# Kernel tuning notes

Hardware: AMD Instinct MI355X
Metric: run time of the kernel (lower is better)

The kernel has to match this reference:

```python
import jax, jax.numpy as jnp
import numpy as np

N = 8192      # nodes
E = 262144    # edges (avg degree 32)
D = 128       # embed dim
F = 128       # input feature dim
H = 128       # GCN hidden
C = 7         # classes
EPS = 1e-4    # sample_bias for concrete noise


def setup_inputs() -> dict:
    key = jax.random.key(0)
    ks = jax.random.split(key, 10)
    x = jax.random.normal(ks[0], (N, F), jnp.float32)
    embed = jax.random.normal(ks[1], (N, D), jnp.float32)
    row = jax.random.randint(ks[2], (E,), 0, N, jnp.int64)
    col = jax.random.randint(ks[3], (E,), 0, N, jnp.int64)
    adj_data = jnp.ones((E,), jnp.float32)
    # uniform noise in (bias, 1-bias) as in concrete_sample(training=True)
    noise = jax.random.uniform(ks[4], (E,), jnp.float32, EPS, 1.0 - EPS)
    tmp = jnp.ones((1,), jnp.float32)  # temperature beta
    W1e = jax.random.normal(ks[5], (3 * D, 64), jnp.float32) * 0.05
    b1e = jnp.zeros((64,), jnp.float32)
    W2e = jax.random.normal(ks[6], (64, 1), jnp.float32) * 0.05
    b2e = jnp.zeros((1,), jnp.float32)
    Wg0 = jax.random.normal(ks[7], (F, H), jnp.float32) * 0.05
    Wg1 = jax.random.normal(ks[8], (H, C), jnp.float32) * 0.05
    return {"x": x, "embed": embed, "adj_data": adj_data, "noise": noise,
            "tmp": tmp, "W1e": W1e, "b1e": b1e, "W2e": W2e, "b2e": b2e,
            "Wg0": Wg0, "Wg1": Wg1, "row": row, "col": col, "nodeid": 5}


def reference(x, embed, adj_data, noise, tmp, W1e, b1e, W2e, b2e, Wg0, Wg1,
              row, col, nodeid):
    # gather node embeddings per edge + self node embedding, concat -> [E, 3D]
    f1 = embed[row]
    f2 = embed[col]
    selfemb = jnp.broadcast_to(embed[nodeid][None, :], (f1.shape[0], D))
    f12self = jnp.concatenate([f1, f2, selfemb], axis=-1)
    # 2-layer explainer MLP -> per-edge logit
    h = jax.nn.relu(f12self @ W1e + b1e)
    log_alpha = (h @ W2e + b2e).reshape(-1)  # [E]
    # concrete-sigmoid reparameterization (training=True path, noise supplied)
    gate_inputs = (jnp.log(noise) - jnp.log1p(-noise) + log_alpha) / tmp[0]
    values = jax.nn.sigmoid(gate_inputs)
    # scatter edge gates and adjacency values into dense [N, N]
    mask = jnp.zeros((N, N), jnp.float32).at[row, col].add(values)
    adj = jnp.zeros((N, N), jnp.float32).at[row, col].add(adj_data)
    # symmetrize mask, apply to adjacency, zero the diagonal
    sym_mask = (mask + mask.T) * 0.5
    masked_adj = adj * sym_mask * (1.0 - jnp.eye(N, dtype=jnp.float32))
    # wrapped GNN: 2-layer GCN
    h1 = jax.nn.relu(masked_adj @ (x @ Wg0))
    out = masked_adj @ (h1 @ Wg1)
    node_pred = out[nodeid]  # [C]
    return jax.nn.softmax(node_pred, axis=0)
```

## Files before the change

kernel.cpp:

```cpp
#include <hip/hip_runtime.h>
#include <hip/hip_bf16.h>
#include <math.h>

#define NNODES 8192
#define DIM 128
#define SMAX 128
#define HSIZE 16384
#define LDAT 136
#define LDW 68

__device__ __forceinline__ int detect64(const void* rowp) {
    const long long* p = (const long long*)rowp;
    int is64 = 1;
#pragma unroll
    for (int i = 0; i < 4; i++) {
        long long v = p[i];
        if (v < 0 || v >= NNODES) is64 = 0;
    }
    return is64;
}

__device__ __forceinline__ int edge_idx(const void* p, int e, int idx64) {
    if (idx64) return (int)((const long long*)p)[e];
    return ((const int*)p)[e];
}

__device__ __forceinline__ int hash_insert(unsigned int* hashK, unsigned int key1) {
    unsigned int h = (key1 * 2654435761u) & (HSIZE - 1);
    for (;;) {
        unsigned int prev = atomicCAS(&hashK[h], 0u, key1);
        if (prev == 0u || prev == key1) return (int)h;
        h = (h + 1) & (HSIZE - 1);
    }
}


__global__ __launch_bounds__(256) void k_zero(float4* z, int n4) {
    int i = blockIdx.x * blockDim.x + threadIdx.x;
    if (i < n4) z[i] = make_float4(0.f, 0.f, 0.f, 0.f);
}

__global__ __launch_bounds__(512) void k_dense(
        const float* embed, const float* x, const float* W1e, const float* b1e,
        const float* Wg0, const int* nodep, const void* rowp, const void* colp,
        const float* adjd,
        float* U, float* V, float* xw, float* cself,
        int* flags, float* cnt0, int* nbr, int* slotmap, int E) {
    int bid = blockIdx.x;
    int t = threadIdx.x;
    int nodeid = nodep[0];
    int tile = bid >> 1;
    int colh = bid & 1;

    __shared__ float At[128 * LDAT];
    __shared__ float Wl[128 * LDW];
    __shared__ float semb[DIM];

    const float* Asrc = (tile < 64) ? embed + (size_t)tile * 128 * DIM
                                    : x + (size_t)(tile - 64) * 128 * DIM;
    for (int i = t; i < 128 * DIM; i += 512)
        At[(i & 127) * LDAT + (i >> 7)] = Asrc[i];
    if (tile < 64) {
        int doff = colh * 128;
        for (int i = t; i < 128 * 64; i += 512)
            Wl[(i >> 6) * LDW + (i & 63)] = W1e[(size_t)(doff + (i >> 6)) * 64 + (i & 63)];
    } else {
        for (int i = t; i < 128 * 64; i += 512)
            Wl[(i >> 6) * LDW + (i & 63)] = Wg0[(size_t)(i >> 6) * DIM + colh * 64 + (i & 63)];
    }
    if (bid == 0 && t < DIM) semb[t] = embed[(size_t)nodeid * DIM + t];
    __syncthreads();

    int rg = t & 31;
    int cg = t >> 5;
    float acc[4][4];
#pragma unroll
    for (int i = 0; i < 4; i++)
#pragma unroll
        for (int j = 0; j < 4; j++) acc[i][j] = 0.f;

#pragma unroll 4
    for (int d = 0; d < DIM; d++) {
        float4 a4 = *(const float4*)&At[d * LDAT + rg * 4];
        float4 w4 = *(const float4*)&Wl[d * LDW + cg * 4];
        const float* ap = &a4.x;
        const float* wp = &w4.x;
#pragma unroll
        for (int i = 0; i < 4; i++)
#pragma unroll
            for (int j = 0; j < 4; j++)
                acc[i][j] = fmaf(ap[i], wp[j], acc[i][j]);
    }

    if (tile < 64) {
        float* o = colh ? V : U;
        int n0 = tile * 128;
#pragma unroll
        for (int i = 0; i < 4; i++)
            *(float4*)&o[(size_t)(n0 + rg * 4 + i) * 64 + cg * 4] =
                make_float4(acc[i][0], acc[i][1], acc[i][2], acc[i][3]);
    } else {
        int n0 = (tile - 64) * 128;
#pragma unroll
        for (int i = 0; i < 4; i++)
            *(float4*)&xw[(size_t)(n0 + rg * 4 + i) * DIM + colh * 64 + cg * 4] =
                make_float4(acc[i][0], acc[i][1], acc[i][2], acc[i][3]);
    }

    if (bid == 0 && t < 64) {
        float a = b1e[t];
        for (int d = 0; d < DIM; d++)
            a += semb[d] * W1e[(size_t)(2 * DIM + d) * 64 + t];
        cself[t] = a;
    }

    int idx64 = detect64(rowp);
    for (int e = bid * 512 + t; e < E; e += 256 * 512) {
        int r = edge_idx(rowp, e, idx64);
        if (r != nodeid) continue;
        int c = edge_idx(colp, e, idx64);
        if (c == nodeid) continue;
        atomicAdd(&cnt0[c], adjd[e]);
        if (atomicCAS((unsigned int*)&slotmap[c], 0u, 0xFFFFFFFFu) == 0u) {
            int s = atomicAdd(&flags[1], 1);
            if (s < SMAX) {
                nbr[s] = c;
                __hip_atomic_store(&slotmap[c], s + 1, __ATOMIC_RELAXED,
                                   __HIP_MEMORY_SCOPE_AGENT);
            }
        }
    }
}

__global__ __launch_bounds__(1024) void k_gates(
        const float* adjd, const float* noise, const float* tmp,
        const float* W2e, const float* b2e,
        const void* rowp, const void* colp, const int* nodep,
        const float* U, const float* V, const float* cself,
        const int* slotmap,
        unsigned int* hashK, float* hashC, float* hashF, float* hashR,
        float* f0s, float* r0s, int E) {
    int idx64 = detect64(rowp);
    int nodeid = nodep[0];
    int e = blockIdx.x * blockDim.x + threadIdx.x;
    if (e >= E) return;
    int r = edge_idx(rowp, e, idx64);
    int c = edge_idx(colp, e, idx64);
    if (r == c) return;
    int spr = slotmap[r];
    int spc = slotmap[c];
    bool fr = spr > 0, fc = spc > 0;
    if (!fr && !fc) return;
    float la = b2e[0];
    const float4* u4 = (const float4*)(U + (size_t)r * 64);
    const float4* v4 = (const float4*)(V + (size_t)c * 64);
    const float4* c4 = (const float4*)cself;
    const float4* w4 = (const float4*)W2e;
#pragma unroll
    for (int d = 0; d < 16; d++) {
        float4 uu = u4[d], vv = v4[d], cc = c4[d], ww = w4[d];
        float h0 = uu.x + vv.x + cc.x;
        float h1 = uu.y + vv.y + cc.y;
        float h2 = uu.z + vv.z + cc.z;
        float h3 = uu.w + vv.w + cc.w;
        la += (h0 > 0.f ? h0 : 0.f) * ww.x + (h1 > 0.f ? h1 : 0.f) * ww.y
            + (h2 > 0.f ? h2 : 0.f) * ww.z + (h3 > 0.f ? h3 : 0.f) * ww.w;
    }
    float nz = noise[e];
    float gi = (logf(nz) - log1pf(-nz) + la) / tmp[0];
    float v = 1.f / (1.f + expf(-gi));
    if (fr) {
        int sr = spr - 1;
        unsigned int key1 = ((unsigned int)(sr << 13) | (unsigned int)c) + 1u;
        int idx = hash_insert(hashK, key1);
        atomicAdd(&hashC[idx], adjd[e]);
        atomicAdd(&hashF[idx], v);
        if (c == nodeid) atomicAdd(&r0s[sr], v);
    }
    if (fc) {
        int sc = spc - 1;
        unsigned int key1 = ((unsigned int)(sc << 13) | (unsigned int)r) + 1u;
        int idx = hash_insert(hashK, key1);
        atomicAdd(&hashR[idx], v);
        if (r == nodeid) atomicAdd(&f0s[sc], v);
    }
}

__global__ __launch_bounds__(1024) void k_hagg(
        const unsigned int* hashK, const float* hashC, const float* hashF,
        const float* hashR, const float* xw, float* h1acc) {
    int gid = blockIdx.x * blockDim.x + threadIdx.x;
    int group = gid >> 7;
    int tg = gid & 127;
    int ngroups = (256 * 1024) >> 7;
    for (int entry = group; entry < HSIZE; entry += ngroups) {
        unsigned int key1 = hashK[entry];
        if (key1 == 0u) continue;
        float wgt = hashC[entry] * (hashF[entry] + hashR[entry]) * 0.5f;
        if (wgt == 0.f) continue;
        unsigned int key = key1 - 1u;
        int s = (int)(key >> 13);
        int k = (int)(key & 8191u);
        atomicAdd(&h1acc[(size_t)s * DIM + tg], wgt * xw[(size_t)k * DIM + tg]);
    }
}

__global__ __launch_bounds__(1024) void k_final(
        const int* flags, const float* h1acc, const float* cnt0, const int* nbr,
        const float* f0s, const float* r0s, const float* Wg1, float* out) {
    int t = threadIdx.x;
    __shared__ float sacc[7];
    if (t < 7) sacc[t] = 0.f;
    __syncthreads();
    int ns = flags[1]; if (ns > SMAX) ns = SMAX;
    int wave = t >> 6, lane = t & 63;
    for (int s = wave; s < ns; s += 16) {
        float a0 = cnt0[nbr[s]] * (f0s[s] + r0s[s]) * 0.5f;
        float v0 = h1acc[(size_t)s * DIM + lane];
        float v1 = h1acc[(size_t)s * DIM + lane + 64];
        v0 = v0 > 0.f ? v0 : 0.f;
        v1 = v1 > 0.f ? v1 : 0.f;
        float part[7];
        for (int c = 0; c < 7; c++) {
            float p = v0 * Wg1[lane * 7 + c] + v1 * Wg1[(lane + 64) * 7 + c];
            for (int o = 32; o >= 1; o >>= 1) p += __shfl_xor(p, o, 64);
            part[c] = p;
        }
        if (lane == 0)
            for (int c = 0; c < 7; c++) atomicAdd(&sacc[c], a0 * part[c]);
    }
    __syncthreads();
    if (t == 0) {
        float v[7], m = -1e30f, ssum = 0.f;
        for (int c = 0; c < 7; c++) { v[c] = sacc[c]; if (v[c] > m) m = v[c]; }
        for (int c = 0; c < 7; c++) { v[c] = expf(v[c] - m); ssum += v[c]; }
        for (int c = 0; c < 7; c++) out[c] = v[c] / ssum;
    }
}

extern "C" void kernel_launch(void* const* d_in, const int* in_sizes, int n_in,
                              void* d_out, int out_size, void* d_ws, size_t ws_size,
                              hipStream_t stream) {
    const float* x     = (const float*)d_in[0];
    const float* embed = (const float*)d_in[1];
    const float* adjd  = (const float*)d_in[2];
    const float* noise = (const float*)d_in[3];
    const float* tmp   = (const float*)d_in[4];
    const float* W1e   = (const float*)d_in[5];
    const float* b1e   = (const float*)d_in[6];
    const float* W2e   = (const float*)d_in[7];
    const float* b2e   = (const float*)d_in[8];
    const float* Wg0   = (const float*)d_in[9];
    const float* Wg1   = (const float*)d_in[10];
    const void*  rowp  = d_in[11];
    const void*  colp  = d_in[12];
    const int*   nodep = (const int*)d_in[13];
    int E = in_sizes[3];

    char* w = (char*)d_ws;
    size_t off = 0;
    auto alloc = [&](size_t bytes) -> char* {
        char* p = w + off;
        off = (off + bytes + 255) & ~(size_t)255;
        return p;
    };
    float*        cself   = (float*)alloc(64 * 4);
    int*          nbr     = (int*)  alloc(SMAX * 4);
    float*        U       = (float*)alloc((size_t)NNODES * 64 * 4);
    float*        V       = (float*)alloc((size_t)NNODES * 64 * 4);
    float*        xw      = (float*)alloc((size_t)NNODES * DIM * 4);
    char*         zstart  = w + off;
    int*          flags   = (int*)  alloc(256);
    int*          slotmap = (int*)  alloc((size_t)NNODES * 4);
    float*        cnt0    = (float*)alloc((size_t)NNODES * 4);
    float*        f0s     = (float*)alloc(SMAX * 4);
    float*        r0s     = (float*)alloc(SMAX * 4);
    unsigned int* hashK   = (unsigned int*)alloc((size_t)HSIZE * 4);
    float*        hashC   = (float*)alloc((size_t)HSIZE * 4);
    float*        hashF   = (float*)alloc((size_t)HSIZE * 4);
    float*        hashR   = (float*)alloc((size_t)HSIZE * 4);
    float*        h1acc   = (float*)alloc((size_t)SMAX * DIM * 4);
    size_t zbytes  = (size_t)((w + off) - zstart);
    int n4 = (int)(zbytes / 16);

    k_zero<<<(n4 + 255) / 256, 256, 0, stream>>>((float4*)zstart, n4);
    k_dense<<<256, 512, 0, stream>>>(embed, x, W1e, b1e, Wg0, nodep, rowp, colp,
                                     adjd, U, V, xw, cself, flags, cnt0, nbr,
                                     slotmap, E);
    k_gates<<<E / 1024, 1024, 0, stream>>>(adjd, noise, tmp, W2e, b2e,
                                           rowp, colp, nodep, U, V, cself,
                                           slotmap, hashK, hashC, hashF, hashR,
                                           f0s, r0s, E);
    k_hagg<<<256, 1024, 0, stream>>>(hashK, hashC, hashF, hashR, xw, h1acc);
    k_final<<<1, 1024, 0, stream>>>(flags, h1acc, cnt0, nbr, f0s, r0s, Wg1,
                                    (float*)d_out);
}
```

Before: 49.33 us.

## Aggregate raw features before Wg0 projection and parallelize final GCN layer

Instead of computing x@Wg0 for all 8192 nodes up front, the hash aggregation now sums raw x rows per neighbor slot, and the final kernel applies Wg0 only to the at most 128 aggregated rows, using one block per slot. This uses linearity to avoid a full dense projection and halves the dense kernel's tile work, which now only computes the explainer U/V with smaller blocks. The hash tables and the aggregation buffer are zeroed inside the dense kernel rather than by k_zero. A last-block-done counter performs the final softmax, which adds a grid-wide atomic handshake.

Measured after the change: 48.21 us. 2.3% less time.

```diff
diff --git a/kernel.cpp b/kernel.cpp
--- a/kernel.cpp
+++ b/kernel.cpp
@@ -6,8 +6,7 @@
 #define DIM 128
 #define SMAX 128
 #define HSIZE 16384
-#define LDAT 136
-#define LDW 68
+#define LDA2 68
 
 __device__ __forceinline__ int detect64(const void* rowp) {
     const long long* p = (const long long*)rowp;
@@ -40,39 +39,36 @@
     if (i < n4) z[i] = make_float4(0.f, 0.f, 0.f, 0.f);
 }
 
-__global__ __launch_bounds__(512) void k_dense(
-        const float* embed, const float* x, const float* W1e, const float* b1e,
-        const float* Wg0, const int* nodep, const void* rowp, const void* colp,
-        const float* adjd,
-        float* U, float* V, float* xw, float* cself,
-        int* flags, float* cnt0, int* nbr, int* slotmap, int E) {
+__global__ __launch_bounds__(256) void k_dense(
+        const float* embed, const float* W1e, const float* b1e,
+        const int* nodep, const void* rowp, const void* colp, const float* adjd,
+        float* U, float* V, float* cself,
+        int* flags, float* cnt0, int* nbr, int* slotmap,
+        float* hzero, int nhz, int E) {
     int bid = blockIdx.x;
     int t = threadIdx.x;
+    int gid = bid * 256 + t;
     int nodeid = nodep[0];
     int tile = bid >> 1;
     int colh = bid & 1;
 
-    __shared__ float At[128 * LDAT];
-    __shared__ float Wl[128 * LDW];
+    __shared__ float At[128 * LDA2];
+    __shared__ float Wl[128 * LDA2];
     __shared__ float semb[DIM];
 
-    const float* Asrc = (tile < 64) ? embed + (size_t)tile * 128 * DIM
-                                    : x + (size_t)(tile - 64) * 128 * DIM;
-    for (int i = t; i < 128 * DIM; i += 512)
-        At[(i & 127) * LDAT + (i >> 7)] = Asrc[i];
-    if (tile < 64) {
-        int doff = colh * 128;
-        for (int i = t; i < 128 * 64; i += 512)
-            Wl[(i >> 6) * LDW + (i & 63)] = W1e[(size_t)(doff + (i >> 6)) * 64 + (i & 63)];
-    } else {
-        for (int i = t; i < 128 * 64; i += 512)
-            Wl[(i >> 6) * LDW + (i & 63)] = Wg0[(size_t)(i >> 6) * DIM + colh * 64 + (i & 63)];
-    }
+    for (int i = gid; i < nhz; i += 256 * 256) hzero[i] = 0.f;
+
+    const float* Asrc = embed + (size_t)tile * 64 * DIM;
+    for (int i = t; i < 64 * DIM; i += 256)
+        At[(i & 127) * LDA2 + (i >> 7)] = Asrc[i];
+    int doff = colh * 128;
+    for (int i = t; i < 128 * 64; i += 256)
+        Wl[(i >> 6) * LDA2 + (i & 63)] = W1e[(size_t)(doff + (i >> 6)) * 64 + (i & 63)];
     if (bid == 0 && t < DIM) semb[t] = embed[(size_t)nodeid * DIM + t];
     __syncthreads();
 
-    int rg = t & 31;
-    int cg = t >> 5;
+    int rg = t & 15;
+    int cg = t >> 4;
     float acc[4][4];
 #pragma unroll
     for (int i = 0; i < 4; i++)
@@ -81,8 +77,8 @@
 
 #pragma unroll 4
     for (int d = 0; d < DIM; d++) {
-        float4 a4 = *(const float4*)&At[d * LDAT + rg * 4];
-        float4 w4 = *(const float4*)&Wl[d * LDW + cg * 4];
+        float4 a4 = *(const float4*)&At[d * LDA2 + rg * 4];
+        float4 w4 = *(const float4*)&Wl[d * LDA2 + cg * 4];
         const float* ap = &a4.x;
         const float* wp = &w4.x;
 #pragma unroll
@@ -92,20 +88,12 @@
                 acc[i][j] = fmaf(ap[i], wp[j], acc[i][j]);
     }
 
-    if (tile < 64) {
-        float* o = colh ? V : U;
-        int n0 = tile * 128;
-#pragma unroll
-        for (int i = 0; i < 4; i++)
-            *(float4*)&o[(size_t)(n0 + rg * 4 + i) * 64 + cg * 4] =
-                make_float4(acc[i][0], acc[i][1], acc[i][2], acc[i][3]);
-    } else {
-        int n0 = (tile - 64) * 128;
-#pragma unroll
-        for (int i = 0; i < 4; i++)
-            *(float4*)&xw[(size_t)(n0 + rg * 4 + i) * DIM + colh * 64 + cg * 4] =
-                make_float4(acc[i][0], acc[i][1], acc[i][2], acc[i][3]);
-    }
+    float* o = colh ? V : U;
+    int n0 = tile * 64;
+#pragma unroll
+    for (int i = 0; i < 4; i++)
+        *(float4*)&o[(size_t)(n0 + rg * 4 + i) * 64 + cg * 4] =
+            make_float4(acc[i][0], acc[i][1], acc[i][2], acc[i][3]);
 
     if (bid == 0 && t < 64) {
         float a = b1e[t];
@@ -115,7 +103,7 @@
     }
 
     int idx64 = detect64(rowp);
-    for (int e = bid * 512 + t; e < E; e += 256 * 512) {
+    for (int e = gid; e < E; e += 256 * 256) {
         int r = edge_idx(rowp, e, idx64);
         if (r != nodeid) continue;
         int c = edge_idx(colp, e, idx64);
@@ -188,7 +176,7 @@
 
 __global__ __launch_bounds__(1024) void k_hagg(
         const unsigned int* hashK, const float* hashC, const float* hashF,
-        const float* hashR, const float* xw, float* h1acc) {
+        const float* hashR, const float* x, float* xagg) {
     int gid = blockIdx.x * blockDim.x + threadIdx.x;
     int group = gid >> 7;
     int tg = gid & 127;
@@ -201,41 +189,59 @@
         unsigned int key = key1 - 1u;
         int s = (int)(key >> 13);
         int k = (int)(key & 8191u);
-        atomicAdd(&h1acc[(size_t)s * DIM + tg], wgt * xw[(size_t)k * DIM + tg]);
-    }
-}
-
-__global__ __launch_bounds__(1024) void k_final(
-        const int* flags, const float* h1acc, const float* cnt0, const int* nbr,
-        const float* f0s, const float* r0s, const float* Wg1, float* out) {
-    int t = threadIdx.x;
-    __shared__ float sacc[7];
-    if (t < 7) sacc[t] = 0.f;
-    __syncthreads();
+        atomicAdd(&xagg[(size_t)s * DIM + tg], wgt * x[(size_t)k * DIM + tg]);
+    }
+}
+
+__global__ __launch_bounds__(128) void k_final(
+        const int* flags, const float* xagg, const float* cnt0, const int* nbr,
+        const float* f0s, const float* r0s, const float* Wg0, const float* Wg1,
+        float* glogits, int* done, float* out) {
+    int b = blockIdx.x, t = threadIdx.x;
     int ns = flags[1]; if (ns > SMAX) ns = SMAX;
-    int wave = t >> 6, lane = t & 63;
-    for (int s = wave; s < ns; s += 16) {
-        float a0 = cnt0[nbr[s]] * (f0s[s] + r0s[s]) * 0.5f;
-        float v0 = h1acc[(size_t)s * DIM + lane];
-        float v1 = h1acc[(size_t)s * DIM + lane + 64];
-        v0 = v0 > 0.f ? v0 : 0.f;
-        v1 = v1 > 0.f ? v1 : 0.f;
+    if (b < ns) {
+        __shared__ float xs[DIM];
+        __shared__ float pacc[2][7];
+        xs[t] = xagg[(size_t)b * DIM + t];
+        __syncthreads();
+        float h = 0.f;
+        for (int d = 0; d < DIM; d++) h = fmaf(xs[d], Wg0[d * DIM + t], h);
+        h = h > 0.f ? h : 0.f;
+        int wave = t >> 6, lane = t & 63;
         float part[7];
         for (int c = 0; c < 7; c++) {
-            float p = v0 * Wg1[lane * 7 + c] + v1 * Wg1[(lane + 64) * 7 + c];
+            float p = h * Wg1[t * 7 + c];
             for (int o = 32; o >= 1; o >>= 1) p += __shfl_xor(p, o, 64);
             part[c] = p;
         }
         if (lane == 0)
-            for (int c = 0; c < 7; c++) atomicAdd(&sacc[c], a0 * part[c]);
+            for (int c = 0; c < 7; c++) pacc[wave][c] = part[c];
+        __syncthreads();
+        if (t == 0) {
+            float a0 = cnt0[nbr[b]] * (f0s[b] + r0s[b]) * 0.5f;
+            for (int c = 0; c < 7; c++)
+                atomicAdd(&glogits[c * 16], a0 * (pacc[0][c] + pacc[1][c]));
+        }
     }
     __syncthreads();
+    __shared__ int lastb;
     if (t == 0) {
-        float v[7], m = -1e30f, ssum = 0.f;
-        for (int c = 0; c < 7; c++) { v[c] = sacc[c]; if (v[c] > m) m = v[c]; }
-        for (int c = 0; c < 7; c++) { v[c] = expf(v[c] - m); ssum += v[c]; }
-        for (int c = 0; c < 7; c++) out[c] = v[c] / ssum;
-    }
+        __threadfence();
+        int old = __hip_atomic_fetch_add(done, 1, __ATOMIC_ACQ_REL,
+                                         __HIP_MEMORY_SCOPE_AGENT);
+        lastb = (old == SMAX - 1) ? 1 : 0;
+    }
+    __syncthreads();
+    if (!lastb || t != 0) return;
+    __builtin_amdgcn_fence(__ATOMIC_ACQUIRE, "agent");
+    float v[7], m = -1e30f, ssum = 0.f;
+    for (int c = 0; c < 7; c++) {
+        v[c] = __hip_atomic_load(&glogits[c * 16], __ATOMIC_RELAXED,
+                                 __HIP_MEMORY_SCOPE_AGENT);
+        if (v[c] > m) m = v[c];
+    }
+    for (int c = 0; c < 7; c++) { v[c] = expf(v[c] - m); ssum += v[c]; }
+    for (int c = 0; c < 7; c++) out[c] = v[c] / ssum;
 }
 
 extern "C" void kernel_launch(void* const* d_in, const int* in_sizes, int n_in,
@@ -268,30 +274,32 @@
     int*          nbr     = (int*)  alloc(SMAX * 4);
     float*        U       = (float*)alloc((size_t)NNODES * 64 * 4);
     float*        V       = (float*)alloc((size_t)NNODES * 64 * 4);
-    float*        xw      = (float*)alloc((size_t)NNODES * DIM * 4);
     char*         zstart  = w + off;
     int*          flags   = (int*)  alloc(256);
+    float*        glogits = (float*)alloc(512);
     int*          slotmap = (int*)  alloc((size_t)NNODES * 4);
     float*        cnt0    = (float*)alloc((size_t)NNODES * 4);
     float*        f0s     = (float*)alloc(SMAX * 4);
     float*        r0s     = (float*)alloc(SMAX * 4);
+    size_t zbytes  = (size_t)((w + off) - zstart);
     unsigned int* hashK   = (unsigned int*)alloc((size_t)HSIZE * 4);
     float*        hashC   = (float*)alloc((size_t)HSIZE * 4);
     float*        hashF   = (float*)alloc((size_t)HSIZE * 4);
     float*        hashR   = (float*)alloc((size_t)HSIZE * 4);
-    float*        h1acc   = (float*)alloc((size_t)SMAX * DIM * 4);
-    size_t zbytes  = (size_t)((w + off) - zstart);
+    float*        xagg    = (float*)alloc((size_t)SMAX * DIM * 4);
+    int nhz = HSIZE * 4 + SMAX * DIM;
     int n4 = (int)(zbytes / 16);
 
     k_zero<<<(n4 + 255) / 256, 256, 0, stream>>>((float4*)zstart, n4);
-    k_dense<<<256, 512, 0, stream>>>(embed, x, W1e, b1e, Wg0, nodep, rowp, colp,
-                                     adjd, U, V, xw, cself, flags, cnt0, nbr,
-                                     slotmap, E);
+    k_dense<<<256, 256, 0, stream>>>(embed, W1e, b1e, nodep, rowp, colp, adjd,
+                                     U, V, cself, flags, cnt0, nbr, slotmap,
+                                     (float*)hashK, nhz, E);
     k_gates<<<E / 1024, 1024, 0, stream>>>(adjd, noise, tmp, W2e, b2e,
                                            rowp, colp, nodep, U, V, cself,
                                            slotmap, hashK, hashC, hashF, hashR,
                                            f0s, r0s, E);
-    k_hagg<<<256, 1024, 0, stream>>>(hashK, hashC, hashF, hashR, xw, h1acc);
-    k_final<<<1, 1024, 0, stream>>>(flags, h1acc, cnt0, nbr, f0s, r0s, Wg1,
-                                    (float*)d_out);
-}
+    k_hagg<<<256, 1024, 0, stream>>>(hashK, hashC, hashF, hashR, x, xagg);
+    k_final<<<SMAX, 128, 0, stream>>>(flags, xagg, cnt0, nbr, f0s, r0s,
+                                      Wg0, Wg1, glogits, &flags[2],
+                                      (float*)d_out);
+}
```
